# Performance work log

Hardware: AMD Instinct MI355X
Metric: run time of the kernel (lower is better)

## Reference

```python
import jax, jax.numpy as jnp
import numpy as np

LEAK = 0.9
BASE_THRESH = 1.0
BN_EPS = 1e-5

@jax.custom_vjp
def spike_fn(x):
    return (x >= 0).astype(x.dtype)

def _spike_fwd(x):
    return (x >= 0).astype(x.dtype), x

def _spike_bwd(x, g):
    return (g / (1.0 + 5.0 * jnp.abs(x)) ** 2,)

spike_fn.defvjp(_spike_fwd, _spike_bwd)


def setup_inputs() -> dict:
    key = jax.random.key(0)
    ks = jax.random.split(key, 8)
    B, T, C, H, NC, DT = 256, 2048, 64, 64, 4, 50
    kin_spikes_seq = jax.random.normal(ks[0], (B, T, C), dtype=jnp.float32)
    tda_features = jax.random.normal(ks[1], (B, DT), dtype=jnp.float32)
    # spatial_conv1x1: Linear(64 -> 64, bias=False); weight [out, in]
    W_spatial = jax.random.normal(ks[2], (H, C), dtype=jnp.float32) / np.sqrt(C)
    bn_gamma = jnp.ones((H,), dtype=jnp.float32)
    bn_beta = jnp.zeros((H,), dtype=jnp.float32)
    # class_conv1x1: Linear(64 -> 4, bias=False)
    W_class = jax.random.normal(ks[3], (NC, H), dtype=jnp.float32) / np.sqrt(H)
    lateral = jnp.eye(NC, dtype=jnp.float32) * 0.8 - 0.1
    # tda_to_thresh: Linear(50 -> 4)
    W_tda = jax.random.normal(ks[4], (NC, DT), dtype=jnp.float32) / np.sqrt(DT)
    b_tda = jnp.zeros((NC,), dtype=jnp.float32)
    return {
        "kin_spikes_seq": kin_spikes_seq,
        "tda_features": tda_features,
        "W_spatial": W_spatial,
        "bn_gamma": bn_gamma,
        "bn_beta": bn_beta,
        "W_class": W_class,
        "lateral": lateral,
        "W_tda": W_tda,
        "b_tda": b_tda,
    }


def reference(kin_spikes_seq, tda_features, W_spatial, bn_gamma, bn_beta,
              W_class, lateral, W_tda, b_tda):
    # [B, T, C] @ [C, H] -> [B, T, H]
    x_proj = jnp.einsum("btc,hc->bth", kin_spikes_seq, W_spatial)
    # BatchNorm1d in training mode: per-channel stats over (B, T)
    mean = jnp.mean(x_proj, axis=(0, 1))
    var = jnp.var(x_proj, axis=(0, 1))
    x_proj = (x_proj - mean) * jax.lax.rsqrt(var + BN_EPS) * bn_gamma + bn_beta

    tda_mod = jax.nn.sigmoid(tda_features @ W_tda.T + b_tda) * 0.5  # [B, 4]
    dynamic_thresh = BASE_THRESH + tda_mod

    B = kin_spikes_seq.shape[0]
    H, NC = W_class.shape[1], W_class.shape[0]
    mem1 = jnp.zeros((B, H), dtype=x_proj.dtype)
    mem2 = jnp.zeros((B, NC), dtype=x_proj.dtype)
    spike_sum = jnp.zeros((B, NC), dtype=x_proj.dtype)

    def step(carry, xt):
        mem1, mem2, ssum = carry
        mem1 = LEAK * mem1 + xt
        spk1 = spike_fn(mem1 - BASE_THRESH)
        mem1 = mem1 * (1.0 - spk1)
        cur2 = (spk1 @ W_class.T) @ lateral  # [B, 4]
        mem2 = LEAK * mem2 + cur2
        spk2 = spike_fn(mem2 - dynamic_thresh)
        mem2 = mem2 * (1.0 - spk2)
        return (mem1, mem2, ssum + spk2), None

    xs = jnp.swapaxes(x_proj, 0, 1)  # [T, B, H]
    (mem1, mem2, spike_sum), _ = jax.lax.scan(step, (mem1, mem2, spike_sum), xs)
    return spike_sum
```

## Files before the change

kernel.cpp:

```cpp
#include <hip/hip_runtime.h>
#include <cstdint>
#include <cstddef>
#include <cmath>

#define BB 256
#define TB 2048
#define NROWS (BB*TB)
#define R1 256
#define NBLK_K1 (NROWS/R1)
#define NBLK1 4096

typedef float f32x4 __attribute__((ext_vector_type(4)));
typedef float f32x2 __attribute__((ext_vector_type(2)));

#define OFF_X      0ull
#define SZ_X       ((size_t)NROWS*64*4)
#define OFF_PART   (OFF_X + SZ_X)
#define SZ_PART    ((size_t)128*NBLK1*4)
#define OFF_STAT   (OFF_PART + SZ_PART)
#define SZ_STAT    (128*8)
#define OFF_MASK   ((OFF_STAT + SZ_STAT + 255ull) & ~255ull)
#define SZ_MASK    ((size_t)NROWS*8)

__global__ __launch_bounds__(256, 2) void k1_gemm(const float* __restrict__ kin,
                                                  const float* __restrict__ Wsp,
                                                  float* __restrict__ xproj,
                                                  float* __restrict__ partials) {
  __shared__ float4 As[R1 * 16];
  __shared__ f32x4 Wp[32 * 32];
  const int tid = threadIdx.x;
  const int ty = tid >> 3;
  const int tx = tid & 7;
  const size_t r0 = (size_t)blockIdx.x * R1;

  const f32x4* kin4 = (const f32x4*)(kin + r0 * 64);
  #pragma unroll
  for (int k = 0; k < 16; ++k) {
    int idx = k * 256 + tid;
    int r = idx >> 4, cc = idx & 15;
    f32x4 v = __builtin_nontemporal_load(&kin4[idx]);
    As[r * 16 + (cc ^ ((r >> 3) & 7))] = make_float4(v.x, v.y, v.z, v.w);
  }
  #pragma unroll
  for (int k = 0; k < 4; ++k) {
    int idx = k * 256 + tid;
    int p = idx >> 5, q = idx & 31;
    float2 w0 = *(const float2*)(Wsp + (2 * p) * 64 + 2 * q);
    float2 w1 = *(const float2*)(Wsp + (2 * p + 1) * 64 + 2 * q);
    Wp[p * 32 + (q ^ ((p >> 2) & 7))] = (f32x4){w0.x, w1.x, w0.y, w1.y};
  }
  __syncthreads();

  f32x2 acc2[8][4];
  #pragma unroll
  for (int i = 0; i < 8; ++i)
    #pragma unroll
    for (int jp = 0; jp < 4; ++jp) acc2[i][jp] = (f32x2){0.f, 0.f};

  #pragma unroll 1
  for (int cc = 0; cc < 16; ++cc) {
    float4 av[8];
    f32x4 q0[4], q1[4];
    #pragma unroll
    for (int i = 0; i < 8; ++i)
      av[i] = As[(8 * ty + i) * 16 + (cc ^ (ty & 7))];
    #pragma unroll
    for (int jp = 0; jp < 4; ++jp) {
      const int p = 4 * tx + jp;
      q0[jp] = Wp[p * 32 + ((2 * cc)     ^ tx)];
      q1[jp] = Wp[p * 32 + ((2 * cc + 1) ^ tx)];
    }
    #pragma unroll
    for (int i = 0; i < 8; ++i) {
      #pragma unroll
      for (int jp = 0; jp < 4; ++jp) {
        acc2[i][jp] = __builtin_elementwise_fma((f32x2){av[i].x, av[i].x}, q0[jp].xy, acc2[i][jp]);
        acc2[i][jp] = __builtin_elementwise_fma((f32x2){av[i].y, av[i].y}, q0[jp].zw, acc2[i][jp]);
        acc2[i][jp] = __builtin_elementwise_fma((f32x2){av[i].z, av[i].z}, q1[jp].xy, acc2[i][jp]);
        acc2[i][jp] = __builtin_elementwise_fma((f32x2){av[i].w, av[i].w}, q1[jp].zw, acc2[i][jp]);
      }
    }
  }

  #pragma unroll
  for (int i = 0; i < 8; ++i) {
    const size_t row = r0 + 8 * ty + i;
    f32x4 lo = {acc2[i][0].x, acc2[i][0].y, acc2[i][1].x, acc2[i][1].y};
    f32x4 hi = {acc2[i][2].x, acc2[i][2].y, acc2[i][3].x, acc2[i][3].y};
    *(f32x4*)(xproj + row * 64 + 8 * tx)     = lo;
    *(f32x4*)(xproj + row * 64 + 8 * tx + 4) = hi;
  }

  __syncthreads();
  float* Sm = (float*)As;
  float* Sq = Sm + 64 * 33;
  #pragma unroll
  for (int j = 0; j < 8; ++j) {
    const int col = 8 * tx + j;
    float s = 0.f, q = 0.f;
    #pragma unroll
    for (int i = 0; i < 8; ++i) {
      float v = (j & 1) ? acc2[i][j >> 1].y : acc2[i][j >> 1].x;
      s += v;
      q += v * v;
    }
    Sm[col * 33 + ty] = s;
    Sq[col * 33 + ty] = q;
  }
  __syncthreads();
  if (tid < 64) {
    float s0 = 0.f, q0 = 0.f, s1 = 0.f, q1 = 0.f;
    #pragma unroll
    for (int g = 0; g < 16; ++g)  { s0 += Sm[tid * 33 + g]; q0 += Sq[tid * 33 + g]; }
    #pragma unroll
    for (int g = 16; g < 32; ++g) { s1 += Sm[tid * 33 + g]; q1 += Sq[tid * 33 + g]; }
    const size_t p0 = 2 * (size_t)blockIdx.x;
    partials[(size_t)tid * NBLK1 + p0]            = s0;
    partials[(size_t)tid * NBLK1 + p0 + 1]        = s1;
    partials[(size_t)(64 + tid) * NBLK1 + p0]     = q0;
    partials[(size_t)(64 + tid) * NBLK1 + p0 + 1] = q1;
  }
}

__global__ __launch_bounds__(256) void k2a_reduce(const float* __restrict__ partials,
                                                  double* __restrict__ statd) {
  __shared__ double sd[256];
  const int idx = blockIdx.x;
  double acc = 0.0;
  for (int k = threadIdx.x; k < NBLK1; k += 256)
    acc += (double)partials[(size_t)idx * NBLK1 + k];
  sd[threadIdx.x] = acc;
  __syncthreads();
  for (int s = 128; s > 0; s >>= 1) {
    if (threadIdx.x < s) sd[threadIdx.x] += sd[threadIdx.x + s];
    __syncthreads();
  }
  if (threadIdx.x == 0) statd[idx] = sd[0];
}

#define K3_LOAD(BUF, TBASE)                         \
  { _Pragma("unroll") for (int i_ = 0; i_ < 64; ++i_) \
      BUF[i_] = xr[(size_t)((TBASE) + i_) * 64]; }

#define K3_CHUNK(CUR, NXT0, TBASE)                                   \
  { unsigned long long keep = 0;                                     \
    _Pragma("unroll") for (int i_ = 0; i_ < 64; ++i_) {              \
      bool sp = (mem >= 1.0f);                                       \
      unsigned long long mb = __ballot(sp);                          \
      if (h == i_) keep = mb;                                        \
      float xrn = (i_ < 63) ? CUR[(i_ + 1) & 63] : (NXT0);           \
      float xn = fmaf(xrn, sc, sh);                                  \
      mem = sp ? xn : fmaf(mem, 0.9f, xn);                           \
    }                                                                \
    masksB[(size_t)b * TB + (TBASE) + h] = keep; }

__global__ __launch_bounds__(64) void k3_scan1(const float* __restrict__ xproj,
                                               const double* __restrict__ statd,
                                               const float* __restrict__ gamma,
                                               const float* __restrict__ beta,
                                               unsigned long long* __restrict__ masksB) {
  const int b = blockIdx.x, h = threadIdx.x;
  const double mean = statd[h] / (double)NROWS;
  const double ex2  = statd[64 + h] / (double)NROWS;
  const double var  = ex2 - mean * mean;
  const double scd  = (double)gamma[h] / sqrt(var + 1e-5);
  const float sc = (float)scd;
  const float sh = (float)((double)beta[h] - mean * scd);

  const float* xr = xproj + (size_t)b * TB * 64 + h;
  float xa[64], xb[64];

  K3_LOAD(xa, 0)
  float mem = fmaf(xa[0], sc, sh);

  #pragma unroll 1
  for (int t0 = 0; t0 < TB; t0 += 128) {
    K3_LOAD(xb, t0 + 64)
    K3_CHUNK(xa, xb[0], t0)
    if (t0 + 128 < TB) { K3_LOAD(xa, t0 + 128) }
    K3_CHUNK(xb, xa[0], t0 + 64)
  }
}

#define K45_LOAD(BUF, TBASE)                                             \
  { _Pragma("unroll") for (int k_ = 0; k_ < 16; ++k_) {                  \
      f32x4 v = *(const f32x4*)(cr + (TBASE) + 4 * k_);                  \
      BUF[4 * k_] = v.x; BUF[4 * k_ + 1] = v.y;                          \
      BUF[4 * k_ + 2] = v.z; BUF[4 * k_ + 3] = v.w; } }

#define K45_CHUNK(CUR, NXT0)                                  \
  { _Pragma("unroll") for (int i_ = 0; i_ < 64; ++i_) {       \
      bool sp = (mem >= th);                                  \
      cnt += sp ? 1u : 0u;                                    \
      float xn = (i_ < 63) ? CUR[(i_ + 1) & 63] : (NXT0);     \
      mem = sp ? xn : fmaf(mem, 0.9f, xn);                    \
    } }

__global__ __launch_bounds__(256) void k45_cur2scan(const unsigned long long* __restrict__ masksB,
                                                    const float* __restrict__ Wc,
                                                    const float* __restrict__ lat,
                                                    const float* __restrict__ tda,
                                                    const float* __restrict__ Wtda,
                                                    const float* __restrict__ btda,
                                                    float* __restrict__ out) {
  __shared__ float WcL[256];
  __shared__ float latL[16];
  __shared__ float thL[4];
  __shared__ float lbuf[4][TB + 4];
  const int tid = threadIdx.x, b = blockIdx.x;
  WcL[tid] = Wc[tid];
  if (tid < 16) latL[tid] = lat[tid];
  if (tid >= 32 && tid < 36) {
    const int j = tid - 32;
    double acc = (double)btda[j];
    for (int k = 0; k < 50; ++k)
      acc += (double)tda[b * 50 + k] * (double)Wtda[j * 50 + k];
    double sig = 1.0 / (1.0 + exp(-acc));
    thL[j] = (float)(1.0 + 0.5 * sig);
  }
  __syncthreads();

  #pragma unroll 1
  for (int c = 0; c < 8; ++c) {
    const int t = c * 256 + tid;
    const unsigned long long m = masksB[(size_t)b * TB + t];
    const unsigned lo = (unsigned)m, hi = (unsigned)(m >> 32);
    float v0 = 0.f, v1 = 0.f, v2 = 0.f, v3 = 0.f;
    #pragma unroll
    for (int hh = 0; hh < 32; ++hh) {
      const float bit = (float)((lo >> hh) & 1u);
      v0 = fmaf(bit, WcL[hh],       v0);
      v1 = fmaf(bit, WcL[64 + hh],  v1);
      v2 = fmaf(bit, WcL[128 + hh], v2);
      v3 = fmaf(bit, WcL[192 + hh], v3);
    }
    #pragma unroll
    for (int hh = 32; hh < 64; ++hh) {
      const float bit = (float)((hi >> (hh - 32)) & 1u);
      v0 = fmaf(bit, WcL[hh],       v0);
      v1 = fmaf(bit, WcL[64 + hh],  v1);
      v2 = fmaf(bit, WcL[128 + hh], v2);
      v3 = fmaf(bit, WcL[192 + hh], v3);
    }
    { float cx = v0 * latL[0];  cx = fmaf(v1, latL[4],  cx); cx = fmaf(v2, latL[8],  cx); cx = fmaf(v3, latL[12], cx); lbuf[0][t] = cx; }
    { float cx = v0 * latL[1];  cx = fmaf(v1, latL[5],  cx); cx = fmaf(v2, latL[9],  cx); cx = fmaf(v3, latL[13], cx); lbuf[1][t] = cx; }
    { float cx = v0 * latL[2];  cx = fmaf(v1, latL[6],  cx); cx = fmaf(v2, latL[10], cx); cx = fmaf(v3, latL[14], cx); lbuf[2][t] = cx; }
    { float cx = v0 * latL[3];  cx = fmaf(v1, latL[7],  cx); cx = fmaf(v2, latL[11], cx); cx = fmaf(v3, latL[15], cx); lbuf[3][t] = cx; }
  }
  __syncthreads();
  if (tid >= 64) return;

  const int j4 = tid & 3;
  const float th = thL[j4];
  const float* cr = lbuf[j4];
  float ca[64], cb[64];

  K45_LOAD(ca, 0)
  float mem = ca[0];
  unsigned cnt = 0;

  #pragma unroll 1
  for (int t0 = 0; t0 < TB; t0 += 128) {
    K45_LOAD(cb, t0 + 64)
    K45_CHUNK(ca, cb[0])
    if (t0 + 128 < TB) { K45_LOAD(ca, t0 + 128) }
    K45_CHUNK(cb, ca[0])
  }
  if (tid < 4) out[b * 4 + j4] = (float)cnt;
}

extern "C" void kernel_launch(void* const* d_in, const int* in_sizes, int n_in,
                              void* d_out, int out_size, void* d_ws, size_t ws_size,
                              hipStream_t stream) {
  const float* kin   = (const float*)d_in[0];
  const float* tda   = (const float*)d_in[1];
  const float* Wsp   = (const float*)d_in[2];
  const float* gamma = (const float*)d_in[3];
  const float* beta  = (const float*)d_in[4];
  const float* Wc    = (const float*)d_in[5];
  const float* lat   = (const float*)d_in[6];
  const float* Wtda  = (const float*)d_in[7];
  const float* btda  = (const float*)d_in[8];

  char* ws = (char*)d_ws;
  float*  xproj    = (float*)(ws + OFF_X);
  float*  partials = (float*)(ws + OFF_PART);
  double* statd    = (double*)(ws + OFF_STAT);
  unsigned long long* masksB = (unsigned long long*)(ws + OFF_MASK);
  float*  out      = (float*)d_out;

  k1_gemm  <<<dim3(NBLK_K1), dim3(256), 0, stream>>>(kin, Wsp, xproj, partials);
  k2a_reduce<<<dim3(128),  dim3(256), 0, stream>>>(partials, statd);
  k3_scan1 <<<dim3(BB),    dim3(64),  0, stream>>>(xproj, statd, gamma, beta, masksB);
  k45_cur2scan<<<dim3(BB), dim3(256), 0, stream>>>(masksB, Wc, lat, tda, Wtda, btda, out);
}
```

Measured before the change: 156.8 us.

## Make GEMM blocks loop over tiles with double-buffered async global-to-LDS loads

The projection GEMM kernel now launches 256 blocks, and each loops over 8 row tiles instead of one block per tile. While the current tile is being computed, the next tile's input is prefetched into a second LDS buffer with direct global-to-LDS loads, using the same swizzled layout. The goal is to hide global load latency behind the FMA work and cut block launch and weight-staging overhead. In exchange, LDS use roughly doubles, occupancy drops to one block (4 waves) per CU, the nontemporal load hint is gone, and each tile gets an extra barrier.

```diff
diff --git a/kernel.cpp b/kernel.cpp
--- a/kernel.cpp
+++ b/kernel.cpp
@@ -7,7 +7,7 @@
 #define TB 2048
 #define NROWS (BB*TB)
 #define R1 256
-#define NBLK_K1 (NROWS/R1)
+#define NTILE 8
 #define NBLK1 4096
 
 typedef float f32x4 __attribute__((ext_vector_type(4)));
@@ -22,24 +22,32 @@
 #define OFF_MASK   ((OFF_STAT + SZ_STAT + 255ull) & ~255ull)
 #define SZ_MASK    ((size_t)NROWS*8)
 
-__global__ __launch_bounds__(256, 2) void k1_gemm(const float* __restrict__ kin,
-                                                  const float* __restrict__ Wsp,
-                                                  float* __restrict__ xproj,
-                                                  float* __restrict__ partials) {
-  __shared__ float4 As[R1 * 16];
+__device__ __forceinline__ void gll16(const float* g, void* l) {
+  __builtin_amdgcn_global_load_lds(
+      (const __attribute__((address_space(1))) unsigned int*)g,
+      (__attribute__((address_space(3))) unsigned int*)l, 16, 0, 0);
+}
+
+__global__ __launch_bounds__(256) void k1_gemm(const float* __restrict__ kin,
+                                               const float* __restrict__ Wsp,
+                                               float* __restrict__ xproj,
+                                               float* __restrict__ partials) {
+  __shared__ float4 Abuf[2][R1 * 16];
   __shared__ f32x4 Wp[32 * 32];
   const int tid = threadIdx.x;
   const int ty = tid >> 3;
   const int tx = tid & 7;
-  const size_t r0 = (size_t)blockIdx.x * R1;
-
-  const f32x4* kin4 = (const f32x4*)(kin + r0 * 64);
-  #pragma unroll
-  for (int k = 0; k < 16; ++k) {
-    int idx = k * 256 + tid;
-    int r = idx >> 4, cc = idx & 15;
-    f32x4 v = __builtin_nontemporal_load(&kin4[idx]);
-    As[r * 16 + (cc ^ ((r >> 3) & 7))] = make_float4(v.x, v.y, v.z, v.w);
+  const size_t blk0 = (size_t)blockIdx.x * NTILE;
+
+  {
+    const float* gA = kin + blk0 * R1 * 64;
+    #pragma unroll
+    for (int k = 0; k < 16; ++k) {
+      const int idx = k * 256 + tid;
+      const int r = idx >> 4, cs = idx & 15;
+      const int gq = cs ^ ((r >> 3) & 7);
+      gll16(gA + (size_t)r * 64 + gq * 4, &Abuf[0][idx]);
+    }
   }
   #pragma unroll
   for (int k = 0; k < 4; ++k) {
@@ -51,74 +59,95 @@
   }
   __syncthreads();
 
-  f32x2 acc2[8][4];
-  #pragma unroll
-  for (int i = 0; i < 8; ++i)
-    #pragma unroll
-    for (int jp = 0; jp < 4; ++jp) acc2[i][jp] = (f32x2){0.f, 0.f};
-
   #pragma unroll 1
-  for (int cc = 0; cc < 16; ++cc) {
-    float4 av[8];
-    f32x4 q0[4], q1[4];
+  for (int t = 0; t < NTILE; ++t) {
+    const int cur = t & 1;
+    const size_t tile = blk0 + t;
+    const size_t r0 = tile * R1;
+
+    if (t + 1 < NTILE) {
+      const float* gA = kin + (r0 + R1) * 64;
+      #pragma unroll
+      for (int k = 0; k < 16; ++k) {
+        const int idx = k * 256 + tid;
+        const int r = idx >> 4, cs = idx & 15;
+        const int gq = cs ^ ((r >> 3) & 7);
+        gll16(gA + (size_t)r * 64 + gq * 4, &Abuf[cur ^ 1][idx]);
+      }
+    }
+
+    const float4* As = Abuf[cur];
+    f32x2 acc2[8][4];
     #pragma unroll
     for (int i = 0; i < 8; ++i)
-      av[i] = As[(8 * ty + i) * 16 + (cc ^ (ty & 7))];
-    #pragma unroll
-    for (int jp = 0; jp < 4; ++jp) {
-      const int p = 4 * tx + jp;
-      q0[jp] = Wp[p * 32 + ((2 * cc)     ^ tx)];
-      q1[jp] = Wp[p * 32 + ((2 * cc + 1) ^ tx)];
-    }
+      #pragma unroll
+      for (int jp = 0; jp < 4; ++jp) acc2[i][jp] = (f32x2){0.f, 0.f};
+
+    #pragma unroll 1
+    for (int cc = 0; cc < 16; ++cc) {
+      float4 av[8];
+      f32x4 q0[4], q1[4];
+      #pragma unroll
+      for (int i = 0; i < 8; ++i)
+        av[i] = As[(8 * ty + i) * 16 + (cc ^ (ty & 7))];
+      #pragma unroll
+      for (int jp = 0; jp < 4; ++jp) {
+        const int p = 4 * tx + jp;
+        q0[jp] = Wp[p * 32 + ((2 * cc)     ^ tx)];
+        q1[jp] = Wp[p * 32 + ((2 * cc + 1) ^ tx)];
+      }
+      #pragma unroll
+      for (int i = 0; i < 8; ++i) {
+        #pragma unroll
+        for (int jp = 0; jp < 4; ++jp) {
+          acc2[i][jp] = __builtin_elementwise_fma((f32x2){av[i].x, av[i].x}, q0[jp].xy, acc2[i][jp]);
+          acc2[i][jp] = __builtin_elementwise_fma((f32x2){av[i].y, av[i].y}, q0[jp].zw, acc2[i][jp]);
+          acc2[i][jp] = __builtin_elementwise_fma((f32x2){av[i].z, av[i].z}, q1[jp].xy, acc2[i][jp]);
+          acc2[i][jp] = __builtin_elementwise_fma((f32x2){av[i].w, av[i].w}, q1[jp].zw, acc2[i][jp]);
+        }
+      }
+    }
+
     #pragma unroll
     for (int i = 0; i < 8; ++i) {
-      #pragma unroll
-      for (int jp = 0; jp < 4; ++jp) {
-        acc2[i][jp] = __builtin_elementwise_fma((f32x2){av[i].x, av[i].x}, q0[jp].xy, acc2[i][jp]);
-        acc2[i][jp] = __builtin_elementwise_fma((f32x2){av[i].y, av[i].y}, q0[jp].zw, acc2[i][jp]);
-        acc2[i][jp] = __builtin_elementwise_fma((f32x2){av[i].z, av[i].z}, q1[jp].xy, acc2[i][jp]);
-        acc2[i][jp] = __builtin_elementwise_fma((f32x2){av[i].w, av[i].w}, q1[jp].zw, acc2[i][jp]);
+      const size_t row = r0 + 8 * ty + i;
+      f32x4 lo = {acc2[i][0].x, acc2[i][0].y, acc2[i][1].x, acc2[i][1].y};
+      f32x4 hi = {acc2[i][2].x, acc2[i][2].y, acc2[i][3].x, acc2[i][3].y};
+      *(f32x4*)(xproj + row * 64 + 8 * tx)     = lo;
+      *(f32x4*)(xproj + row * 64 + 8 * tx + 4) = hi;
+    }
+
+    __syncthreads();
+
+    float* Sm = (float*)Abuf[cur];
+    float* Sq = Sm + 64 * 33;
+    #pragma unroll
+    for (int j = 0; j < 8; ++j) {
+      const int col = 8 * tx + j;
+      float s = 0.f, q = 0.f;
+      #pragma unroll
+      for (int i = 0; i < 8; ++i) {
+        float v = (j & 1) ? acc2[i][j >> 1].y : acc2[i][j >> 1].x;
+        s += v;
+        q += v * v;
       }
-    }
-  }
-
-  #pragma unroll
-  for (int i = 0; i < 8; ++i) {
-    const size_t row = r0 + 8 * ty + i;
-    f32x4 lo = {acc2[i][0].x, acc2[i][0].y, acc2[i][1].x, acc2[i][1].y};
-    f32x4 hi = {acc2[i][2].x, acc2[i][2].y, acc2[i][3].x, acc2[i][3].y};
-    *(f32x4*)(xproj + row * 64 + 8 * tx)     = lo;
-    *(f32x4*)(xproj + row * 64 + 8 * tx + 4) = hi;
-  }
-
-  __syncthreads();
-  float* Sm = (float*)As;
-  float* Sq = Sm + 64 * 33;
-  #pragma unroll
-  for (int j = 0; j < 8; ++j) {
-    const int col = 8 * tx + j;
-    float s = 0.f, q = 0.f;
-    #pragma unroll
-    for (int i = 0; i < 8; ++i) {
-      float v = (j & 1) ? acc2[i][j >> 1].y : acc2[i][j >> 1].x;
-      s += v;
-      q += v * v;
-    }
-    Sm[col * 33 + ty] = s;
-    Sq[col * 33 + ty] = q;
-  }
-  __syncthreads();
-  if (tid < 64) {
-    float s0 = 0.f, q0 = 0.f, s1 = 0.f, q1 = 0.f;
-    #pragma unroll
-    for (int g = 0; g < 16; ++g)  { s0 += Sm[tid * 33 + g]; q0 += Sq[tid * 33 + g]; }
-    #pragma unroll
-    for (int g = 16; g < 32; ++g) { s1 += Sm[tid * 33 + g]; q1 += Sq[tid * 33 + g]; }
-    const size_t p0 = 2 * (size_t)blockIdx.x;
-    partials[(size_t)tid * NBLK1 + p0]            = s0;
-    partials[(size_t)tid * NBLK1 + p0 + 1]        = s1;
-    partials[(size_t)(64 + tid) * NBLK1 + p0]     = q0;
-    partials[(size_t)(64 + tid) * NBLK1 + p0 + 1] = q1;
+      Sm[col * 33 + ty] = s;
+      Sq[col * 33 + ty] = q;
+    }
+    __syncthreads();
+    if (tid < 64) {
+      float s0 = 0.f, q0 = 0.f, s1 = 0.f, q1 = 0.f;
+      #pragma unroll
+      for (int g = 0; g < 16; ++g)  { s0 += Sm[tid * 33 + g]; q0 += Sq[tid * 33 + g]; }
+      #pragma unroll
+      for (int g = 16; g < 32; ++g) { s1 += Sm[tid * 33 + g]; q1 += Sq[tid * 33 + g]; }
+      const size_t p0 = 2 * tile;
+      partials[(size_t)tid * NBLK1 + p0]            = s0;
+      partials[(size_t)tid * NBLK1 + p0 + 1]        = s1;
+      partials[(size_t)(64 + tid) * NBLK1 + p0]     = q0;
+      partials[(size_t)(64 + tid) * NBLK1 + p0 + 1] = q1;
+    }
+    __syncthreads();
   }
 }
 
@@ -289,7 +318,7 @@
   unsigned long long* masksB = (unsigned long long*)(ws + OFF_MASK);
   float*  out      = (float*)d_out;
 
-  k1_gemm  <<<dim3(NBLK_K1), dim3(256), 0, stream>>>(kin, Wsp, xproj, partials);
+  k1_gemm  <<<dim3(256),   dim3(256), 0, stream>>>(kin, Wsp, xproj, partials);
   k2a_reduce<<<dim3(128),  dim3(256), 0, stream>>>(partials, statd);
   k3_scan1 <<<dim3(BB),    dim3(64),  0, stream>>>(xproj, statd, gamma, beta, masksB);
   k45_cur2scan<<<dim3(BB), dim3(256), 0, stream>>>(masksB, Wc, lat, tda, Wtda, btda, out);
```

Measured after the change: 181.5 us. 15.7% more time.

## Make projection GEMM persistent with double-buffered direct-to-LDS async loads

Applied to the files above, without the earlier changes.

The projection GEMM becomes a persistent-style kernel. Each of 512 blocks of 128 threads walks 8 tiles of 128 rows, double-buffering the input tiles in shared memory through global_load_lds DMA, with manual vmcnt waits so the next tile's load overlaps the current tile's FMA work. The goal is to hide global-load latency and skip the register round trip when staging the input. The trade-offs are lower occupancy per block, more barriers per tile, and a fragile hand-counted waitcnt scheme. The per-block partial statistics layout is kept at 4096 entries per channel.

```diff
diff --git a/kernel.cpp b/kernel.cpp
--- a/kernel.cpp
+++ b/kernel.cpp
@@ -6,8 +6,9 @@
 #define BB 256
 #define TB 2048
 #define NROWS (BB*TB)
-#define R1 256
-#define NBLK_K1 (NROWS/R1)
+#define RT 128
+#define NT1 8
+#define GRID1 512
 #define NBLK1 4096
 
 typedef float f32x4 __attribute__((ext_vector_type(4)));
@@ -22,28 +23,28 @@
 #define OFF_MASK   ((OFF_STAT + SZ_STAT + 255ull) & ~255ull)
 #define SZ_MASK    ((size_t)NROWS*8)
 
-__global__ __launch_bounds__(256, 2) void k1_gemm(const float* __restrict__ kin,
-                                                  const float* __restrict__ Wsp,
-                                                  float* __restrict__ xproj,
-                                                  float* __restrict__ partials) {
-  __shared__ float4 As[R1 * 16];
+__device__ __forceinline__ void gll16(const float* g, void* l) {
+  __builtin_amdgcn_global_load_lds(
+      (const __attribute__((address_space(1))) unsigned int*)g,
+      (__attribute__((address_space(3))) unsigned int*)l, 16, 0, 0);
+}
+
+__global__ __launch_bounds__(128) void k1_gemm(const float* __restrict__ kin,
+                                               const float* __restrict__ Wsp,
+                                               float* __restrict__ xproj,
+                                               float* __restrict__ partials) {
+  __shared__ float4 Abuf[2][RT * 16];
   __shared__ f32x4 Wp[32 * 32];
   const int tid = threadIdx.x;
   const int ty = tid >> 3;
   const int tx = tid & 7;
-  const size_t r0 = (size_t)blockIdx.x * R1;
-
-  const f32x4* kin4 = (const f32x4*)(kin + r0 * 64);
+  const int wv = tid >> 6;
+  const int lt = tid & 63;
+  const size_t row0 = (size_t)blockIdx.x * (NT1 * RT);
+
   #pragma unroll
-  for (int k = 0; k < 16; ++k) {
-    int idx = k * 256 + tid;
-    int r = idx >> 4, cc = idx & 15;
-    f32x4 v = __builtin_nontemporal_load(&kin4[idx]);
-    As[r * 16 + (cc ^ ((r >> 3) & 7))] = make_float4(v.x, v.y, v.z, v.w);
-  }
-  #pragma unroll
-  for (int k = 0; k < 4; ++k) {
-    int idx = k * 256 + tid;
+  for (int k = 0; k < 8; ++k) {
+    int idx = k * 128 + tid;
     int p = idx >> 5, q = idx & 31;
     float2 w0 = *(const float2*)(Wsp + (2 * p) * 64 + 2 * q);
     float2 w1 = *(const float2*)(Wsp + (2 * p + 1) * 64 + 2 * q);
@@ -51,75 +52,103 @@
   }
   __syncthreads();
 
-  f32x2 acc2[8][4];
+#define ISSUE_A(TT, BB_)                                                     \
+  { const float* gA = kin + (row0 + (size_t)(TT) * RT) * 64;                 \
+    _Pragma("unroll") for (int k_ = 0; k_ < 16; ++k_) {                      \
+      const int idx = wv * 1024 + k_ * 64 + lt;                              \
+      const int r_ = idx >> 4, cs_ = idx & 15;                               \
+      const int gq_ = cs_ ^ ((r_ >> 3) & 7);                                 \
+      gll16(gA + (size_t)r_ * 64 + gq_ * 4, &Abuf[BB_][idx]);                \
+    } }
+
+  ISSUE_A(0, 0)
+
   #pragma unroll
-  for (int i = 0; i < 8; ++i)
-    #pragma unroll
-    for (int jp = 0; jp < 4; ++jp) acc2[i][jp] = (f32x2){0.f, 0.f};
-
-  #pragma unroll 1
-  for (int cc = 0; cc < 16; ++cc) {
-    float4 av[8];
-    f32x4 q0[4], q1[4];
+  for (int t = 0; t < NT1; ++t) {
+    const int cur = t & 1;
+    if (t + 1 < NT1) ISSUE_A(t + 1, cur ^ 1)
+
+    if (t == 0 || t == NT1 - 1) {
+      asm volatile("s_waitcnt vmcnt(16)" ::: "memory");
+    } else {
+      asm volatile("s_waitcnt vmcnt(32)" ::: "memory");
+    }
+
+    const float4* As = Abuf[cur];
+    f32x2 acc2[8][4];
     #pragma unroll
     for (int i = 0; i < 8; ++i)
-      av[i] = As[(8 * ty + i) * 16 + (cc ^ (ty & 7))];
-    #pragma unroll
-    for (int jp = 0; jp < 4; ++jp) {
-      const int p = 4 * tx + jp;
-      q0[jp] = Wp[p * 32 + ((2 * cc)     ^ tx)];
-      q1[jp] = Wp[p * 32 + ((2 * cc + 1) ^ tx)];
-    }
+      #pragma unroll
+      for (int jp = 0; jp < 4; ++jp) acc2[i][jp] = (f32x2){0.f, 0.f};
+
+    #pragma unroll 1
+    for (int cc = 0; cc < 16; ++cc) {
+      float4 av[8];
+      f32x4 q0[4], q1[4];
+      #pragma unroll
+      for (int i = 0; i < 8; ++i)
+        av[i] = As[(8 * ty + i) * 16 + (cc ^ (ty & 7))];
+      #pragma unroll
+      for (int jp = 0; jp < 4; ++jp) {
+        const int p = 4 * tx + jp;
+        q0[jp] = Wp[p * 32 + ((2 * cc)     ^ tx)];
+        q1[jp] = Wp[p * 32 + ((2 * cc + 1) ^ tx)];
+      }
+      #pragma unroll
+      for (int i = 0; i < 8; ++i) {
+        #pragma unroll
+        for (int jp = 0; jp < 4; ++jp) {
+          acc2[i][jp] = __builtin_elementwise_fma((f32x2){av[i].x, av[i].x}, q0[jp].xy, acc2[i][jp]);
+          acc2[i][jp] = __builtin_elementwise_fma((f32x2){av[i].y, av[i].y}, q0[jp].zw, acc2[i][jp]);
+          acc2[i][jp] = __builtin_elementwise_fma((f32x2){av[i].z, av[i].z}, q1[jp].xy, acc2[i][jp]);
+          acc2[i][jp] = __builtin_elementwise_fma((f32x2){av[i].w, av[i].w}, q1[jp].zw, acc2[i][jp]);
+        }
+      }
+    }
+
+    const size_t tile_r0 = row0 + (size_t)t * RT;
     #pragma unroll
     for (int i = 0; i < 8; ++i) {
-      #pragma unroll
-      for (int jp = 0; jp < 4; ++jp) {
-        acc2[i][jp] = __builtin_elementwise_fma((f32x2){av[i].x, av[i].x}, q0[jp].xy, acc2[i][jp]);
-        acc2[i][jp] = __builtin_elementwise_fma((f32x2){av[i].y, av[i].y}, q0[jp].zw, acc2[i][jp]);
-        acc2[i][jp] = __builtin_elementwise_fma((f32x2){av[i].z, av[i].z}, q1[jp].xy, acc2[i][jp]);
-        acc2[i][jp] = __builtin_elementwise_fma((f32x2){av[i].w, av[i].w}, q1[jp].zw, acc2[i][jp]);
+      const size_t row = tile_r0 + 8 * ty + i;
+      f32x4 lo = {acc2[i][0].x, acc2[i][0].y, acc2[i][1].x, acc2[i][1].y};
+      f32x4 hi = {acc2[i][2].x, acc2[i][2].y, acc2[i][3].x, acc2[i][3].y};
+      *(f32x4*)(xproj + row * 64 + 8 * tx)     = lo;
+      *(f32x4*)(xproj + row * 64 + 8 * tx + 4) = hi;
+    }
+
+    __builtin_amdgcn_s_barrier();
+    float* Sm = (float*)Abuf[cur];
+    float* Sq = Sm + 64 * 17;
+    #pragma unroll
+    for (int j = 0; j < 8; ++j) {
+      const int col = 8 * tx + j;
+      float s = 0.f, q = 0.f;
+      #pragma unroll
+      for (int i = 0; i < 8; ++i) {
+        float v = (j & 1) ? acc2[i][j >> 1].y : acc2[i][j >> 1].x;
+        s += v;
+        q += v * v;
       }
-    }
-  }
-
-  #pragma unroll
-  for (int i = 0; i < 8; ++i) {
-    const size_t row = r0 + 8 * ty + i;
-    f32x4 lo = {acc2[i][0].x, acc2[i][0].y, acc2[i][1].x, acc2[i][1].y};
-    f32x4 hi = {acc2[i][2].x, acc2[i][2].y, acc2[i][3].x, acc2[i][3].y};
-    *(f32x4*)(xproj + row * 64 + 8 * tx)     = lo;
-    *(f32x4*)(xproj + row * 64 + 8 * tx + 4) = hi;
-  }
-
-  __syncthreads();
-  float* Sm = (float*)As;
-  float* Sq = Sm + 64 * 33;
-  #pragma unroll
-  for (int j = 0; j < 8; ++j) {
-    const int col = 8 * tx + j;
-    float s = 0.f, q = 0.f;
-    #pragma unroll
-    for (int i = 0; i < 8; ++i) {
-      float v = (j & 1) ? acc2[i][j >> 1].y : acc2[i][j >> 1].x;
-      s += v;
-      q += v * v;
-    }
-    Sm[col * 33 + ty] = s;
-    Sq[col * 33 + ty] = q;
-  }
-  __syncthreads();
-  if (tid < 64) {
-    float s0 = 0.f, q0 = 0.f, s1 = 0.f, q1 = 0.f;
-    #pragma unroll
-    for (int g = 0; g < 16; ++g)  { s0 += Sm[tid * 33 + g]; q0 += Sq[tid * 33 + g]; }
-    #pragma unroll
-    for (int g = 16; g < 32; ++g) { s1 += Sm[tid * 33 + g]; q1 += Sq[tid * 33 + g]; }
-    const size_t p0 = 2 * (size_t)blockIdx.x;
-    partials[(size_t)tid * NBLK1 + p0]            = s0;
-    partials[(size_t)tid * NBLK1 + p0 + 1]        = s1;
-    partials[(size_t)(64 + tid) * NBLK1 + p0]     = q0;
-    partials[(size_t)(64 + tid) * NBLK1 + p0 + 1] = q1;
-  }
+      Sm[col * 17 + ty] = s;
+      Sq[col * 17 + ty] = q;
+    }
+    asm volatile("s_waitcnt lgkmcnt(0)" ::: "memory");
+    __builtin_amdgcn_s_barrier();
+    if (tid < 64) {
+      float s = 0.f, q = 0.f;
+      #pragma unroll
+      for (int g = 0; g < 16; ++g) {
+        s += Sm[tid * 17 + g];
+        q += Sq[tid * 17 + g];
+      }
+      const size_t pg = (size_t)blockIdx.x * NT1 + t;
+      partials[(size_t)tid * NBLK1 + pg]        = s;
+      partials[(size_t)(64 + tid) * NBLK1 + pg] = q;
+    }
+    asm volatile("s_waitcnt lgkmcnt(0)" ::: "memory");
+    __builtin_amdgcn_s_barrier();
+  }
+#undef ISSUE_A
 }
 
 __global__ __launch_bounds__(256) void k2a_reduce(const float* __restrict__ partials,
@@ -289,8 +318,8 @@
   unsigned long long* masksB = (unsigned long long*)(ws + OFF_MASK);
   float*  out      = (float*)d_out;
 
-  k1_gemm  <<<dim3(NBLK_K1), dim3(256), 0, stream>>>(kin, Wsp, xproj, partials);
-  k2a_reduce<<<dim3(128),  dim3(256), 0, stream>>>(partials, statd);
-  k3_scan1 <<<dim3(BB),    dim3(64),  0, stream>>>(xproj, statd, gamma, beta, masksB);
-  k45_cur2scan<<<dim3(BB), dim3(256), 0, stream>>>(masksB, Wc, lat, tda, Wtda, btda, out);
-}
+  k1_gemm  <<<dim3(GRID1),  dim3(128), 0, stream>>>(kin, Wsp, xproj, partials);
+  k2a_reduce<<<dim3(128),   dim3(256), 0, stream>>>(partials, statd);
+  k3_scan1 <<<dim3(BB),     dim3(64),  0, stream>>>(xproj, statd, gamma, beta, masksB);
+  k45_cur2scan<<<dim3(BB),  dim3(256), 0, stream>>>(masksB, Wc, lat, tda, Wtda, btda, out);
+}
```

Measured after the change: 179.3 us. 1.14x slower.

## Rewrite projection GEMM with weights in registers and broadcast row loads

Applied to the files above, without the earlier changes.

The projection GEMM no longer stages inputs and weights in LDS. Each lane now keeps one output channel's 64 weights in registers, and each wave streams its 256 rows through double-buffered register loads. Because every lane reads the same input address, those loads act as broadcasts. The kernel launches 512 blocks, each covering 1024 rows, and writes BN partial sums per 128 rows straight from registers, which removes the shared-memory reduction and its barriers. In exchange it uses many more registers per thread, has less parallelism, and puts more load instructions on the uniform-address path.

```diff
diff --git a/kernel.cpp b/kernel.cpp
--- a/kernel.cpp
+++ b/kernel.cpp
@@ -6,12 +6,9 @@
 #define BB 256
 #define TB 2048
 #define NROWS (BB*TB)
-#define R1 256
-#define NBLK_K1 (NROWS/R1)
 #define NBLK1 4096
 
 typedef float f32x4 __attribute__((ext_vector_type(4)));
-typedef float f32x2 __attribute__((ext_vector_type(2)));
 
 #define OFF_X      0ull
 #define SZ_X       ((size_t)NROWS*64*4)
@@ -22,103 +19,81 @@
 #define OFF_MASK   ((OFF_STAT + SZ_STAT + 255ull) & ~255ull)
 #define SZ_MASK    ((size_t)NROWS*8)
 
-__global__ __launch_bounds__(256, 2) void k1_gemm(const float* __restrict__ kin,
-                                                  const float* __restrict__ Wsp,
-                                                  float* __restrict__ xproj,
-                                                  float* __restrict__ partials) {
-  __shared__ float4 As[R1 * 16];
-  __shared__ f32x4 Wp[32 * 32];
-  const int tid = threadIdx.x;
-  const int ty = tid >> 3;
-  const int tx = tid & 7;
-  const size_t r0 = (size_t)blockIdx.x * R1;
-
-  const f32x4* kin4 = (const f32x4*)(kin + r0 * 64);
+__global__ __launch_bounds__(256) void k1_gemm(const float* __restrict__ kin,
+                                               const float* __restrict__ Wsp,
+                                               float* __restrict__ xproj,
+                                               float* __restrict__ partials) {
+  const int lane = threadIdx.x & 63;
+  const int wv = __builtin_amdgcn_readfirstlane((int)(threadIdx.x >> 6));
+
+  float wreg[64];
+  {
+    const float4* ws = (const float4*)(Wsp + lane * 64);
+    #pragma unroll
+    for (int k = 0; k < 16; ++k) {
+      float4 v = ws[k];
+      wreg[4*k] = v.x; wreg[4*k+1] = v.y; wreg[4*k+2] = v.z; wreg[4*k+3] = v.w;
+    }
+  }
+
+  const size_t rowbase = (size_t)blockIdx.x * 1024 + (size_t)wv * 256;
+  const float* A = kin + rowbase * 64;
+  float* X = xproj + rowbase * 64;
+
+  float4 abuf[2][8];
   #pragma unroll
-  for (int k = 0; k < 16; ++k) {
-    int idx = k * 256 + tid;
-    int r = idx >> 4, cc = idx & 15;
-    f32x4 v = __builtin_nontemporal_load(&kin4[idx]);
-    As[r * 16 + (cc ^ ((r >> 3) & 7))] = make_float4(v.x, v.y, v.z, v.w);
-  }
-  #pragma unroll
-  for (int k = 0; k < 4; ++k) {
-    int idx = k * 256 + tid;
-    int p = idx >> 5, q = idx & 31;
-    float2 w0 = *(const float2*)(Wsp + (2 * p) * 64 + 2 * q);
-    float2 w1 = *(const float2*)(Wsp + (2 * p + 1) * 64 + 2 * q);
-    Wp[p * 32 + (q ^ ((p >> 2) & 7))] = (f32x4){w0.x, w1.x, w0.y, w1.y};
-  }
-  __syncthreads();
-
-  f32x2 acc2[8][4];
-  #pragma unroll
-  for (int i = 0; i < 8; ++i)
-    #pragma unroll
-    for (int jp = 0; jp < 4; ++jp) acc2[i][jp] = (f32x2){0.f, 0.f};
-
-  #pragma unroll 1
-  for (int cc = 0; cc < 16; ++cc) {
-    float4 av[8];
-    f32x4 q0[4], q1[4];
-    #pragma unroll
-    for (int i = 0; i < 8; ++i)
-      av[i] = As[(8 * ty + i) * 16 + (cc ^ (ty & 7))];
-    #pragma unroll
-    for (int jp = 0; jp < 4; ++jp) {
-      const int p = 4 * tx + jp;
-      q0[jp] = Wp[p * 32 + ((2 * cc)     ^ tx)];
-      q1[jp] = Wp[p * 32 + ((2 * cc + 1) ^ tx)];
-    }
-    #pragma unroll
-    for (int i = 0; i < 8; ++i) {
+  for (int r = 0; r < 8; ++r)
+    abuf[0][r] = *(const float4*)(A + r * 64);
+
+  float psum = 0.f, pq = 0.f;
+
+  #pragma unroll 1
+  for (int g = 0; g < 32; ++g) {
+    float acc[8];
+    #pragma unroll
+    for (int r = 0; r < 8; ++r) acc[r] = 0.f;
+
+    #pragma unroll
+    for (int cc = 0; cc < 16; ++cc) {
+      const int cur = cc & 1;
+      if (cc < 15) {
+        #pragma unroll
+        for (int r = 0; r < 8; ++r)
+          abuf[cur ^ 1][r] = *(const float4*)(A + (g * 8 + r) * 64 + (cc + 1) * 4);
+      } else if (g < 31) {
+        #pragma unroll
+        for (int r = 0; r < 8; ++r)
+          abuf[cur ^ 1][r] = *(const float4*)(A + ((g + 1) * 8 + r) * 64);
+      }
       #pragma unroll
-      for (int jp = 0; jp < 4; ++jp) {
-        acc2[i][jp] = __builtin_elementwise_fma((f32x2){av[i].x, av[i].x}, q0[jp].xy, acc2[i][jp]);
-        acc2[i][jp] = __builtin_elementwise_fma((f32x2){av[i].y, av[i].y}, q0[jp].zw, acc2[i][jp]);
-        acc2[i][jp] = __builtin_elementwise_fma((f32x2){av[i].z, av[i].z}, q1[jp].xy, acc2[i][jp]);
-        acc2[i][jp] = __builtin_elementwise_fma((f32x2){av[i].w, av[i].w}, q1[jp].zw, acc2[i][jp]);
+      for (int r = 0; r < 8; ++r) {
+        float4 a = abuf[cur][r];
+        acc[r] = fmaf(a.x, wreg[4*cc],     acc[r]);
+        acc[r] = fmaf(a.y, wreg[4*cc + 1], acc[r]);
+        acc[r] = fmaf(a.z, wreg[4*cc + 2], acc[r]);
+        acc[r] = fmaf(a.w, wreg[4*cc + 3], acc[r]);
       }
     }
-  }
-
-  #pragma unroll
-  for (int i = 0; i < 8; ++i) {
-    const size_t row = r0 + 8 * ty + i;
-    f32x4 lo = {acc2[i][0].x, acc2[i][0].y, acc2[i][1].x, acc2[i][1].y};
-    f32x4 hi = {acc2[i][2].x, acc2[i][2].y, acc2[i][3].x, acc2[i][3].y};
-    *(f32x4*)(xproj + row * 64 + 8 * tx)     = lo;
-    *(f32x4*)(xproj + row * 64 + 8 * tx + 4) = hi;
-  }
-
-  __syncthreads();
-  float* Sm = (float*)As;
-  float* Sq = Sm + 64 * 33;
-  #pragma unroll
-  for (int j = 0; j < 8; ++j) {
-    const int col = 8 * tx + j;
+
+    #pragma unroll
+    for (int r = 0; r < 8; ++r)
+      X[(g * 8 + r) * 64 + lane] = acc[r];
+
     float s = 0.f, q = 0.f;
     #pragma unroll
-    for (int i = 0; i < 8; ++i) {
-      float v = (j & 1) ? acc2[i][j >> 1].y : acc2[i][j >> 1].x;
-      s += v;
-      q += v * v;
-    }
-    Sm[col * 33 + ty] = s;
-    Sq[col * 33 + ty] = q;
-  }
-  __syncthreads();
-  if (tid < 64) {
-    float s0 = 0.f, q0 = 0.f, s1 = 0.f, q1 = 0.f;
-    #pragma unroll
-    for (int g = 0; g < 16; ++g)  { s0 += Sm[tid * 33 + g]; q0 += Sq[tid * 33 + g]; }
-    #pragma unroll
-    for (int g = 16; g < 32; ++g) { s1 += Sm[tid * 33 + g]; q1 += Sq[tid * 33 + g]; }
-    const size_t p0 = 2 * (size_t)blockIdx.x;
-    partials[(size_t)tid * NBLK1 + p0]            = s0;
-    partials[(size_t)tid * NBLK1 + p0 + 1]        = s1;
-    partials[(size_t)(64 + tid) * NBLK1 + p0]     = q0;
-    partials[(size_t)(64 + tid) * NBLK1 + p0 + 1] = q1;
+    for (int r = 0; r < 8; ++r) {
+      s += acc[r];
+      q += acc[r] * acc[r];
+    }
+    psum += s;
+    pq   += q;
+
+    if ((g & 15) == 15) {
+      const size_t pg = (rowbase >> 7) + (g >> 4);
+      partials[(size_t)lane * NBLK1 + pg]        = psum;
+      partials[(size_t)(64 + lane) * NBLK1 + pg] = pq;
+      psum = 0.f; pq = 0.f;
+    }
   }
 }
 
@@ -289,7 +264,7 @@
   unsigned long long* masksB = (unsigned long long*)(ws + OFF_MASK);
   float*  out      = (float*)d_out;
 
-  k1_gemm  <<<dim3(NBLK_K1), dim3(256), 0, stream>>>(kin, Wsp, xproj, partials);
+  k1_gemm  <<<dim3(512),   dim3(256), 0, stream>>>(kin, Wsp, xproj, partials);
   k2a_reduce<<<dim3(128),  dim3(256), 0, stream>>>(partials, statd);
   k3_scan1 <<<dim3(BB),    dim3(64),  0, stream>>>(xproj, statd, gamma, beta, masksB);
   k45_cur2scan<<<dim3(BB), dim3(256), 0, stream>>>(masksB, Wc, lat, tda, Wtda, btda, out);
```

After: 567.9 us. 3.62x slower.
